# Optimization experiments

Hardware: AMD Instinct MI355X
Metric: run time of the kernel (lower is better)

The kernel has to match this reference:

```python
import jax, jax.numpy as jnp
import numpy as np

B, N, C, O, K = 8, 1024, 64, 64, 3  # batch, nodes, in_c, out_c, Cheb order
EPS = 1e-12


def setup_inputs() -> dict:
    key = jax.random.key(0)
    ks = jax.random.split(key, 10)
    X_real = jax.random.normal(ks[0], (B, N, C), dtype=jnp.float32)
    X_imag = jax.random.normal(ks[1], (B, N, C), dtype=jnp.float32)
    L_real = jax.random.normal(ks[2], (B, K + 1, N, N), dtype=jnp.float32)
    L_imag = jax.random.normal(ks[3], (B, K + 1, N, N), dtype=jnp.float32)
    # Chebyshev weights: uniform(-stdv, stdv) then normalized to unit complex magnitude (as in __init__)
    stdv = 1.0 / np.sqrt(O)
    w_real = jax.random.uniform(ks[4], (K + 1, C, O), minval=-stdv, maxval=stdv, dtype=jnp.float32)
    w_imag = jax.random.uniform(ks[5], (K + 1, C, O), minval=-stdv, maxval=stdv, dtype=jnp.float32)
    mag = jnp.sqrt(w_real ** 2 + w_imag ** 2)
    w_real = w_real / mag
    w_imag = w_imag / mag
    # complex attention linear: maps 2*C -> 1
    a_stdv = 1.0 / np.sqrt(2 * C)
    attn_w_real = jax.random.uniform(ks[6], (2 * C,), minval=-a_stdv, maxval=a_stdv, dtype=jnp.float32)
    attn_w_imag = jax.random.uniform(ks[7], (2 * C,), minval=-a_stdv, maxval=a_stdv, dtype=jnp.float32)
    attn_b_real = jnp.zeros((1,), dtype=jnp.float32)
    attn_b_imag = jnp.zeros((1,), dtype=jnp.float32)
    # complex PReLU slopes (PyTorch PReLU default init 0.25)
    prelu_a_real = jnp.full((1,), 0.25, dtype=jnp.float32)
    prelu_a_imag = jnp.full((1,), 0.25, dtype=jnp.float32)
    return dict(X_real=X_real, X_imag=X_imag, L_real=L_real, L_imag=L_imag,
                w_real=w_real, w_imag=w_imag,
                attn_w_real=attn_w_real, attn_w_imag=attn_w_imag,
                attn_b_real=attn_b_real, attn_b_imag=attn_b_imag,
                prelu_a_real=prelu_a_real, prelu_a_imag=prelu_a_imag)


def reference(X_real, X_imag, L_real, L_imag, w_real, w_imag,
              attn_w_real, attn_w_imag, attn_b_real, attn_b_imag,
              prelu_a_real, prelu_a_imag):
    c = X_real.shape[-1]
    # --- attention scores: CVLinear on concat(x_i, x_j) decomposes into per-node terms ---
    Wr_i, Wr_j = attn_w_real[:c], attn_w_real[c:]
    Wi_i, Wi_j = attn_w_imag[:c], attn_w_imag[c:]
    sR_i = X_real @ Wr_i - X_imag @ Wi_i  # [B,N]
    sI_i = X_real @ Wi_i + X_imag @ Wr_i
    sR_j = X_real @ Wr_j - X_imag @ Wi_j
    sI_j = X_real @ Wi_j + X_imag @ Wr_j
    scores_r = sR_i[:, :, None] + sR_j[:, None, :] + attn_b_real  # [B,N,N]
    scores_i = sI_i[:, :, None] + sI_j[:, None, :] + attn_b_imag
    # --- complex PReLU (applied to real/imag separately) ---
    pr = jnp.where(scores_r >= 0, scores_r, prelu_a_real * scores_r)
    pi = jnp.where(scores_i >= 0, scores_i, prelu_a_imag * scores_i)
    # --- phase softmax over dim=1: softmax of magnitude, phase preserved ---
    mag = jnp.sqrt(pr ** 2 + pi ** 2)
    sm = jax.nn.softmax(mag, axis=1)
    scale = sm / (mag + EPS)
    ar = scale * pr  # [B,N,N] complex attention (real part)
    ai = scale * pi
    # --- modulate complex Laplacian stack [B,K+1,N,N] ---
    Lr = L_real * ar[:, None] - L_imag * ai[:, None]
    Li = L_real * ai[:, None] + L_imag * ar[:, None]
    # einsum 'bijk,bqjp->bijp' with q-size 1 == rowsum over k, then scale X per node j
    rowR = Lr.sum(-1)  # [B,K+1,N]
    rowI = Li.sum(-1)
    # complex (L-rowsum * X) @ W, summed over the K+1 terms (torch.sum dim=2 of stack)
    real = (jnp.einsum('bmj,bjc,mco->bjo', rowR, X_real, w_real)
            - jnp.einsum('bmj,bjc,mco->bjo', rowI, X_imag, w_imag))
    imag = (jnp.einsum('bmj,bjc,mco->bjo', rowI, X_real, w_real)
            + jnp.einsum('bmj,bjc,mco->bjo', rowR, X_imag, w_imag))
    return real, imag
```

## Files before the change

kernel.cpp:

```cpp
#include <hip/hip_runtime.h>

#define EPS_Q 1e-12f

typedef float nfloat4 __attribute__((ext_vector_type(4)));

__device__ __forceinline__ float wave_reduce_sum(float v) {
#pragma unroll
    for (int m = 32; m > 0; m >>= 1) v += __shfl_xor(v, m, 64);
    return v;
}

__global__ __launch_bounds__(256)
void k_scores(const float* __restrict__ Xr, const float* __restrict__ Xi,
              const float* __restrict__ awr, const float* __restrict__ awi,
              float* __restrict__ sRi, float* __restrict__ sIi,
              float* __restrict__ sRj, float* __restrict__ sIj) {
    const int lane = threadIdx.x & 63;
    const int row  = (blockIdx.x << 2) + (threadIdx.x >> 6);
    const float xr = Xr[row * 64 + lane];
    const float xi = Xi[row * 64 + lane];
    const float wri = awr[lane], wrj = awr[64 + lane];
    const float wii = awi[lane], wij = awi[64 + lane];
    float v0 = xr * wri - xi * wii;
    float v1 = xr * wii + xi * wri;
    float v2 = xr * wrj - xi * wij;
    float v3 = xr * wij + xi * wrj;
#pragma unroll
    for (int m = 32; m > 0; m >>= 1) {
        v0 += __shfl_xor(v0, m, 64);
        v1 += __shfl_xor(v1, m, 64);
        v2 += __shfl_xor(v2, m, 64);
        v3 += __shfl_xor(v3, m, 64);
    }
    if (lane == 0) {
        sRi[row] = v0;
        sIi[row] = v1;
        sRj[row] = v2;
        sIj[row] = v3;
    }
}

__global__ __launch_bounds__(256)
void k_softmax(const float* __restrict__ sRi, const float* __restrict__ sIi,
               const float* __restrict__ sRj, const float* __restrict__ sIj,
               float* __restrict__ cmax, float* __restrict__ cinv,
               const float* __restrict__ abr, const float* __restrict__ abi,
               const float* __restrict__ par_, const float* __restrict__ pai_) {
    const int lane = threadIdx.x & 63;
    const int row  = (blockIdx.x << 2) + (threadIdx.x >> 6);
    const int b    = row >> 10;
    const float br = abr[0], bi = abi[0], par = par_[0], pai = pai_[0];
    const float sRjv = sRj[row], sIjv = sIj[row];
    const float* pR = sRi + (b << 10);
    const float* pI = sIi + (b << 10);
    float mags[16];
    float mx = -3.4e38f;
#pragma unroll
    for (int t = 0; t < 16; ++t) {
        const int i = (t << 6) + lane;
        float sr = pR[i] + sRjv + br;
        float si = pI[i] + sIjv + bi;
        float pr = sr >= 0.f ? sr : par * sr;
        float pi = si >= 0.f ? si : pai * si;
        float mg = sqrtf(pr * pr + pi * pi);
        mags[t] = mg;
        mx = fmaxf(mx, mg);
    }
#pragma unroll
    for (int m = 32; m > 0; m >>= 1) mx = fmaxf(mx, __shfl_xor(mx, m, 64));
    float s = 0.f;
#pragma unroll
    for (int t = 0; t < 16; ++t) s += __expf(mags[t] - mx);
    s = wave_reduce_sum(s);
    if (lane == 0) {
        cmax[row] = mx;
        cinv[row] = 1.f / s;
    }
}

__device__ __forceinline__ void attn_coef(float srj, float sij, float mx, float is,
                                          float sri, float sii,
                                          float br, float bi, float par, float pai,
                                          float& ar, float& ai) {
    float sr = sri + srj + br;
    float si = sii + sij + bi;
    float pr = sr >= 0.f ? sr : par * sr;
    float pi = si >= 0.f ? si : pai * si;
    float mg = sqrtf(pr * pr + pi * pi);
    float sc = __expf(mg - mx) * is / (mg + EPS_Q);
    ar = sc * pr;
    ai = sc * pi;
}

#define FMA_BURST(m, R, Q)                                              \
    {                                                                   \
        _Pragma("unroll")                                               \
        for (int t = 0; t < 4; ++t) {                                   \
            accR[m] += R[t].x * arv[(t << 2) + 0] - Q[t].x * aiv[(t << 2) + 0]; \
            accI[m] += R[t].x * aiv[(t << 2) + 0] + Q[t].x * arv[(t << 2) + 0]; \
            accR[m] += R[t].y * arv[(t << 2) + 1] - Q[t].y * aiv[(t << 2) + 1]; \
            accI[m] += R[t].y * aiv[(t << 2) + 1] + Q[t].y * arv[(t << 2) + 1]; \
            accR[m] += R[t].z * arv[(t << 2) + 2] - Q[t].z * aiv[(t << 2) + 2]; \
            accI[m] += R[t].z * aiv[(t << 2) + 2] + Q[t].z * arv[(t << 2) + 2]; \
            accR[m] += R[t].w * arv[(t << 2) + 3] - Q[t].w * aiv[(t << 2) + 3]; \
            accI[m] += R[t].w * aiv[(t << 2) + 3] + Q[t].w * arv[(t << 2) + 3]; \
        }                                                               \
    }

#define LOAD_BURST(m, R, Q)                                             \
    {                                                                   \
        _Pragma("unroll")                                               \
        for (int t = 0; t < 4; ++t) {                                   \
            R[t] = __builtin_nontemporal_load(&LR[((m) << 18) + (t << 6) + lane]); \
            Q[t] = __builtin_nontemporal_load(&LI[((m) << 18) + (t << 6) + lane]); \
        }                                                               \
    }

__global__ __launch_bounds__(256)
void k_stream_out(const float* __restrict__ Lr, const float* __restrict__ Li,
                  const float* __restrict__ sRi, const float* __restrict__ sIi,
                  const float* __restrict__ sRj, const float* __restrict__ sIj,
                  const float* __restrict__ cmax, const float* __restrict__ cinv,
                  const float* __restrict__ abr, const float* __restrict__ abi,
                  const float* __restrict__ par_, const float* __restrict__ pai_,
                  const float* __restrict__ Xr, const float* __restrict__ Xi,
                  const float* __restrict__ wr, const float* __restrict__ wi,
                  float* __restrict__ out) {
    __shared__ float luR[4][4][64];
    __shared__ float luI[4][4][64];
    const int lane = threadIdx.x & 63;
    const int wave = threadIdx.x >> 6;
    const int wid  = (blockIdx.x << 2) + wave;
    const int b    = wid >> 10;
    const int i    = wid & 1023;
    const float br = abr[0], bi = abi[0], par = par_[0], pai = pai_[0];
    const float sri = sRi[wid], sii = sIi[wid];

    const float4* SRJ = (const float4*)(sRj + (b << 10));
    const float4* SIJ = (const float4*)(sIj + (b << 10));
    const float4* CMX = (const float4*)(cmax + (b << 10));
    const float4* CIV = (const float4*)(cinv + (b << 10));

    float arv[16], aiv[16];
#pragma unroll
    for (int t = 0; t < 4; ++t) {
        const int j4 = (t << 6) + lane;
        const float4 vr = SRJ[j4];
        const float4 vi = SIJ[j4];
        const float4 vm = CMX[j4];
        const float4 vs = CIV[j4];
        attn_coef(vr.x, vi.x, vm.x, vs.x, sri, sii, br, bi, par, pai,
                  arv[(t << 2) + 0], aiv[(t << 2) + 0]);
        attn_coef(vr.y, vi.y, vm.y, vs.y, sri, sii, br, bi, par, pai,
                  arv[(t << 2) + 1], aiv[(t << 2) + 1]);
        attn_coef(vr.z, vi.z, vm.z, vs.z, sri, sii, br, bi, par, pai,
                  arv[(t << 2) + 2], aiv[(t << 2) + 2]);
        attn_coef(vr.w, vi.w, vm.w, vs.w, sri, sii, br, bi, par, pai,
                  arv[(t << 2) + 3], aiv[(t << 2) + 3]);
    }

    const size_t base = ((size_t)b << 22) + ((size_t)i << 10);
    const nfloat4* LR = (const nfloat4*)(Lr + base);
    const nfloat4* LI = (const nfloat4*)(Li + base);

    float accR[4] = {0.f, 0.f, 0.f, 0.f};
    float accI[4] = {0.f, 0.f, 0.f, 0.f};
    nfloat4 rA[4], qA[4], rB[4], qB[4];
    LOAD_BURST(0, rA, qA);
    LOAD_BURST(1, rB, qB);
    FMA_BURST(0, rA, qA);
    LOAD_BURST(2, rA, qA);
    FMA_BURST(1, rB, qB);
    LOAD_BURST(3, rB, qB);
    FMA_BURST(2, rA, qA);
    FMA_BURST(3, rB, qB);

#pragma unroll
    for (int m = 0; m < 4; ++m) {
#pragma unroll
        for (int s = 32; s > 0; s >>= 1) {
            accR[m] += __shfl_xor(accR[m], s, 64);
            accI[m] += __shfl_xor(accI[m], s, 64);
        }
    }

    const int row0 = blockIdx.x << 2;
    float xrv[4], xiv[4];
#pragma unroll
    for (int r = 0; r < 4; ++r) {
        xrv[r] = Xr[(size_t)(row0 + r) * 64 + lane];
        xiv[r] = Xi[(size_t)(row0 + r) * 64 + lane];
    }
    float u[4] = {0.f, 0.f, 0.f, 0.f};
    float v[4] = {0.f, 0.f, 0.f, 0.f};
#pragma unroll 4
    for (int c = 0; c < 64; ++c) {
        const float wrv = wr[(((wave << 6) + c) << 6) + lane];
        const float wiv = wi[(((wave << 6) + c) << 6) + lane];
#pragma unroll
        for (int r = 0; r < 4; ++r) {
            u[r] += __shfl(xrv[r], c, 64) * wrv;
            v[r] += __shfl(xiv[r], c, 64) * wiv;
        }
    }
#pragma unroll
    for (int r = 0; r < 4; ++r) {
        luR[wave][r][lane] = u[r];
        luI[wave][r][lane] = v[r];
    }
    __syncthreads();
    float re = 0.f, im = 0.f;
#pragma unroll
    for (int m = 0; m < 4; ++m) {
        const float um = luR[m][wave][lane];
        const float vm = luI[m][wave][lane];
        re += accR[m] * um - accI[m] * vm;
        im += accI[m] * um + accR[m] * vm;
    }
    out[(size_t)wid * 64 + lane] = re;
    out[524288 + (size_t)wid * 64 + lane] = im;
}

extern "C" void kernel_launch(void* const* d_in, const int* in_sizes, int n_in,
                              void* d_out, int out_size, void* d_ws, size_t ws_size,
                              hipStream_t stream) {
    const float* Xr  = (const float*)d_in[0];
    const float* Xi  = (const float*)d_in[1];
    const float* Lr  = (const float*)d_in[2];
    const float* Li  = (const float*)d_in[3];
    const float* wr  = (const float*)d_in[4];
    const float* wi  = (const float*)d_in[5];
    const float* awr = (const float*)d_in[6];
    const float* awi = (const float*)d_in[7];
    const float* abr = (const float*)d_in[8];
    const float* abi = (const float*)d_in[9];
    const float* par = (const float*)d_in[10];
    const float* pai = (const float*)d_in[11];
    float* out = (float*)d_out;

    float* ws   = (float*)d_ws;
    float* sRi  = ws;
    float* sIi  = ws + 8192;
    float* sRj  = ws + 16384;
    float* sIj  = ws + 24576;
    float* cmax = ws + 32768;
    float* cinv = ws + 40960;

    k_scores    <<<dim3(2048), dim3(256), 0, stream>>>(Xr, Xi, awr, awi, sRi, sIi, sRj, sIj);
    k_softmax   <<<dim3(2048), dim3(256), 0, stream>>>(sRi, sIi, sRj, sIj, cmax, cinv,
                                                       abr, abi, par, pai);
    k_stream_out<<<dim3(2048), dim3(256), 0, stream>>>(Lr, Li, sRi, sIi, sRj, sIj, cmax, cinv,
                                                       abr, abi, par, pai,
                                                       Xr, Xi, wr, wi, out);
}
```

Measured before the change: 309.5 us.

## Precompute X·W products in scores kernel and issue first L loads earlier

Moves the per-node X@W products (u, v for all K+1 terms) out of the bandwidth-bound streaming kernel into the first kernel. That kernel now stages 16 rows of X in LDS and writes U/V as float4 per node to workspace. The streaming kernel drops its shuffle-based matmul, shared memory and block barrier, issues the first L load burst before computing attention coefficients, and reads precomputed U/V late. This adds about 16 MB of workspace writes and reads in exchange for removing compute and a sync from the hot streaming kernel.

```diff
diff --git a/kernel.cpp b/kernel.cpp
--- a/kernel.cpp
+++ b/kernel.cpp
@@ -11,32 +11,82 @@
 }
 
 __global__ __launch_bounds__(256)
-void k_scores(const float* __restrict__ Xr, const float* __restrict__ Xi,
-              const float* __restrict__ awr, const float* __restrict__ awi,
-              float* __restrict__ sRi, float* __restrict__ sIi,
-              float* __restrict__ sRj, float* __restrict__ sIj) {
-    const int lane = threadIdx.x & 63;
-    const int row  = (blockIdx.x << 2) + (threadIdx.x >> 6);
-    const float xr = Xr[row * 64 + lane];
-    const float xi = Xi[row * 64 + lane];
-    const float wri = awr[lane], wrj = awr[64 + lane];
-    const float wii = awi[lane], wij = awi[64 + lane];
-    float v0 = xr * wri - xi * wii;
-    float v1 = xr * wii + xi * wri;
-    float v2 = xr * wrj - xi * wij;
-    float v3 = xr * wij + xi * wrj;
-#pragma unroll
-    for (int m = 32; m > 0; m >>= 1) {
-        v0 += __shfl_xor(v0, m, 64);
-        v1 += __shfl_xor(v1, m, 64);
-        v2 += __shfl_xor(v2, m, 64);
-        v3 += __shfl_xor(v3, m, 64);
-    }
-    if (lane == 0) {
-        sRi[row] = v0;
-        sIi[row] = v1;
-        sRj[row] = v2;
-        sIj[row] = v3;
+void k_scores_uv(const float* __restrict__ Xr, const float* __restrict__ Xi,
+                 const float* __restrict__ awr, const float* __restrict__ awi,
+                 const float* __restrict__ wr, const float* __restrict__ wi,
+                 float* __restrict__ sRi, float* __restrict__ sIi,
+                 float* __restrict__ sRj, float* __restrict__ sIj,
+                 float4* __restrict__ U4, float4* __restrict__ V4) {
+    __shared__ float lxr[16][64];
+    __shared__ float lxi[16][64];
+    const int tid = threadIdx.x;
+    const int rb  = blockIdx.x << 4;
+    {
+        const float4* s0 = (const float4*)(Xr + (size_t)rb * 64);
+        const float4* s1 = (const float4*)(Xi + (size_t)rb * 64);
+        ((float4*)&lxr[0][0])[tid] = s0[tid];
+        ((float4*)&lxi[0][0])[tid] = s1[tid];
+    }
+    __syncthreads();
+    const int wave = tid >> 6, lane = tid & 63;
+    const int r0 = wave << 2;
+
+    {
+        const float wri = awr[lane], wrj = awr[64 + lane];
+        const float wii = awi[lane], wij = awi[64 + lane];
+#pragma unroll
+        for (int r = 0; r < 4; ++r) {
+            const int row = rb + r0 + r;
+            const float xr = lxr[r0 + r][lane];
+            const float xi = lxi[r0 + r][lane];
+            float v0 = xr * wri - xi * wii;
+            float v1 = xr * wii + xi * wri;
+            float v2 = xr * wrj - xi * wij;
+            float v3 = xr * wij + xi * wrj;
+#pragma unroll
+            for (int m = 32; m > 0; m >>= 1) {
+                v0 += __shfl_xor(v0, m, 64);
+                v1 += __shfl_xor(v1, m, 64);
+                v2 += __shfl_xor(v2, m, 64);
+                v3 += __shfl_xor(v3, m, 64);
+            }
+            if (lane == 0) {
+                sRi[row] = v0;
+                sIi[row] = v1;
+                sRj[row] = v2;
+                sIj[row] = v3;
+            }
+        }
+    }
+
+    float u[4][4], v[4][4];
+#pragma unroll
+    for (int r = 0; r < 4; ++r)
+#pragma unroll
+        for (int m = 0; m < 4; ++m) { u[r][m] = 0.f; v[r][m] = 0.f; }
+    for (int c = 0; c < 64; ++c) {
+        float wrv[4], wiv[4];
+#pragma unroll
+        for (int m = 0; m < 4; ++m) {
+            wrv[m] = wr[((m << 6) + c) * 64 + lane];
+            wiv[m] = wi[((m << 6) + c) * 64 + lane];
+        }
+#pragma unroll
+        for (int r = 0; r < 4; ++r) {
+            const float xr = lxr[r0 + r][c];
+            const float xi = lxi[r0 + r][c];
+#pragma unroll
+            for (int m = 0; m < 4; ++m) {
+                u[r][m] += xr * wrv[m];
+                v[r][m] += xi * wiv[m];
+            }
+        }
+    }
+#pragma unroll
+    for (int r = 0; r < 4; ++r) {
+        const int row = rb + r0 + r;
+        U4[(row << 6) + lane] = make_float4(u[r][0], u[r][1], u[r][2], u[r][3]);
+        V4[(row << 6) + lane] = make_float4(v[r][0], v[r][1], v[r][2], v[r][3]);
     }
 }
 
@@ -117,30 +167,33 @@
     }
 
 __global__ __launch_bounds__(256)
-void k_stream_out(const float* __restrict__ Lr, const float* __restrict__ Li,
-                  const float* __restrict__ sRi, const float* __restrict__ sIi,
-                  const float* __restrict__ sRj, const float* __restrict__ sIj,
-                  const float* __restrict__ cmax, const float* __restrict__ cinv,
-                  const float* __restrict__ abr, const float* __restrict__ abi,
-                  const float* __restrict__ par_, const float* __restrict__ pai_,
-                  const float* __restrict__ Xr, const float* __restrict__ Xi,
-                  const float* __restrict__ wr, const float* __restrict__ wi,
-                  float* __restrict__ out) {
-    __shared__ float luR[4][4][64];
-    __shared__ float luI[4][4][64];
+void k_stream(const float* __restrict__ Lr, const float* __restrict__ Li,
+              const float* __restrict__ sRi, const float* __restrict__ sIi,
+              const float* __restrict__ sRj, const float* __restrict__ sIj,
+              const float* __restrict__ cmax, const float* __restrict__ cinv,
+              const float* __restrict__ abr, const float* __restrict__ abi,
+              const float* __restrict__ par_, const float* __restrict__ pai_,
+              const float4* __restrict__ U4, const float4* __restrict__ V4,
+              float* __restrict__ out) {
     const int lane = threadIdx.x & 63;
     const int wave = threadIdx.x >> 6;
     const int wid  = (blockIdx.x << 2) + wave;
     const int b    = wid >> 10;
     const int i    = wid & 1023;
+
+    const size_t base = ((size_t)b << 22) + ((size_t)i << 10);
+    const nfloat4* LR = (const nfloat4*)(Lr + base);
+    const nfloat4* LI = (const nfloat4*)(Li + base);
+
+    nfloat4 rA[4], qA[4], rB[4], qB[4];
+    LOAD_BURST(0, rA, qA);
+
     const float br = abr[0], bi = abi[0], par = par_[0], pai = pai_[0];
     const float sri = sRi[wid], sii = sIi[wid];
-
     const float4* SRJ = (const float4*)(sRj + (b << 10));
     const float4* SIJ = (const float4*)(sIj + (b << 10));
     const float4* CMX = (const float4*)(cmax + (b << 10));
     const float4* CIV = (const float4*)(cinv + (b << 10));
-
     float arv[16], aiv[16];
 #pragma unroll
     for (int t = 0; t < 4; ++t) {
@@ -159,20 +212,16 @@
                   arv[(t << 2) + 3], aiv[(t << 2) + 3]);
     }
 
-    const size_t base = ((size_t)b << 22) + ((size_t)i << 10);
-    const nfloat4* LR = (const nfloat4*)(Lr + base);
-    const nfloat4* LI = (const nfloat4*)(Li + base);
-
     float accR[4] = {0.f, 0.f, 0.f, 0.f};
     float accI[4] = {0.f, 0.f, 0.f, 0.f};
-    nfloat4 rA[4], qA[4], rB[4], qB[4];
-    LOAD_BURST(0, rA, qA);
     LOAD_BURST(1, rB, qB);
     FMA_BURST(0, rA, qA);
     LOAD_BURST(2, rA, qA);
     FMA_BURST(1, rB, qB);
     LOAD_BURST(3, rB, qB);
     FMA_BURST(2, rA, qA);
+    const float4 uR = U4[(wid << 6) + lane];
+    const float4 vI = V4[(wid << 6) + lane];
     FMA_BURST(3, rB, qB);
 
 #pragma unroll
@@ -184,39 +233,11 @@
         }
     }
 
-    const int row0 = blockIdx.x << 2;
-    float xrv[4], xiv[4];
-#pragma unroll
-    for (int r = 0; r < 4; ++r) {
-        xrv[r] = Xr[(size_t)(row0 + r) * 64 + lane];
-        xiv[r] = Xi[(size_t)(row0 + r) * 64 + lane];
-    }
-    float u[4] = {0.f, 0.f, 0.f, 0.f};
-    float v[4] = {0.f, 0.f, 0.f, 0.f};
-#pragma unroll 4
-    for (int c = 0; c < 64; ++c) {
-        const float wrv = wr[(((wave << 6) + c) << 6) + lane];
-        const float wiv = wi[(((wave << 6) + c) << 6) + lane];
-#pragma unroll
-        for (int r = 0; r < 4; ++r) {
-            u[r] += __shfl(xrv[r], c, 64) * wrv;
-            v[r] += __shfl(xiv[r], c, 64) * wiv;
-        }
-    }
-#pragma unroll
-    for (int r = 0; r < 4; ++r) {
-        luR[wave][r][lane] = u[r];
-        luI[wave][r][lane] = v[r];
-    }
-    __syncthreads();
     float re = 0.f, im = 0.f;
-#pragma unroll
-    for (int m = 0; m < 4; ++m) {
-        const float um = luR[m][wave][lane];
-        const float vm = luI[m][wave][lane];
-        re += accR[m] * um - accI[m] * vm;
-        im += accI[m] * um + accR[m] * vm;
-    }
+    re += accR[0] * uR.x - accI[0] * vI.x;  im += accI[0] * uR.x + accR[0] * vI.x;
+    re += accR[1] * uR.y - accI[1] * vI.y;  im += accI[1] * uR.y + accR[1] * vI.y;
+    re += accR[2] * uR.z - accI[2] * vI.z;  im += accI[2] * uR.z + accR[2] * vI.z;
+    re += accR[3] * uR.w - accI[3] * vI.w;  im += accI[3] * uR.w + accR[3] * vI.w;
     out[(size_t)wid * 64 + lane] = re;
     out[524288 + (size_t)wid * 64 + lane] = im;
 }
@@ -238,18 +259,20 @@
     const float* pai = (const float*)d_in[11];
     float* out = (float*)d_out;
 
-    float* ws   = (float*)d_ws;
-    float* sRi  = ws;
-    float* sIi  = ws + 8192;
-    float* sRj  = ws + 16384;
-    float* sIj  = ws + 24576;
-    float* cmax = ws + 32768;
-    float* cinv = ws + 40960;
-
-    k_scores    <<<dim3(2048), dim3(256), 0, stream>>>(Xr, Xi, awr, awi, sRi, sIi, sRj, sIj);
-    k_softmax   <<<dim3(2048), dim3(256), 0, stream>>>(sRi, sIi, sRj, sIj, cmax, cinv,
-                                                       abr, abi, par, pai);
-    k_stream_out<<<dim3(2048), dim3(256), 0, stream>>>(Lr, Li, sRi, sIi, sRj, sIj, cmax, cinv,
-                                                       abr, abi, par, pai,
-                                                       Xr, Xi, wr, wi, out);
-}
+    float*  ws   = (float*)d_ws;
+    float*  sRi  = ws;
+    float*  sIi  = ws + 8192;
+    float*  sRj  = ws + 16384;
+    float*  sIj  = ws + 24576;
+    float*  cmax = ws + 32768;
+    float*  cinv = ws + 40960;
+    float4* U4   = (float4*)(ws + 49152);
+    float4* V4   = (float4*)(ws + 49152 + 2097152);
+
+    k_scores_uv<<<dim3(512),  dim3(256), 0, stream>>>(Xr, Xi, awr, awi, wr, wi,
+                                                      sRi, sIi, sRj, sIj, U4, V4);
+    k_softmax  <<<dim3(2048), dim3(256), 0, stream>>>(sRi, sIi, sRj, sIj, cmax, cinv,
+                                                      abr, abi, par, pai);
+    k_stream   <<<dim3(2048), dim3(256), 0, stream>>>(Lr, Li, sRi, sIi, sRj, sIj, cmax, cinv,
+                                                      abr, abi, par, pai, U4, V4, out);
+}
```

New measurement: 325.0 us. +5.0%, slower.
